# Kernel optimization log

Measured on AMD Instinct MI355X. Metric: run time of the kernel, lower is better.

Reference implementation:

```python
import jax, jax.numpy as jnp
import numpy as np

B = 131072
GI, GO = 4, 4          # input/output pathway groups
NI, NO = 64, 32        # neurons per input group (256/4), per output group (128/4)


def _gelu(t):
    # torch F.gelu default = exact erf gelu
    return jax.nn.gelu(t, approximate=False)


def setup_inputs() -> dict:
    key = jax.random.key(0)
    ks = jax.random.split(key, 16)
    s = 0.02
    return {
        "x":  jax.random.normal(ks[0], (B, 784), jnp.float32),
        "W1": jax.random.normal(ks[1], (512, 784), jnp.float32) * s,
        "b1": jax.random.normal(ks[2], (512,), jnp.float32) * s,
        "W2": jax.random.normal(ks[3], (256, 512), jnp.float32) * s,
        "b2": jax.random.normal(ks[4], (256,), jnp.float32) * s,
        "W3": jax.random.normal(ks[5], (128, 256), jnp.float32) * s,
        "b3": jax.random.normal(ks[6], (128,), jnp.float32) * s,
        "W4": jax.random.normal(ks[7], (64, 128), jnp.float32) * s,
        "b4": jax.random.normal(ks[8], (64,), jnp.float32) * s,
        "W5": jax.random.normal(ks[9], (32, 64), jnp.float32) * s,
        "b5": jax.random.normal(ks[10], (32,), jnp.float32) * s,
        "W6": jax.random.normal(ks[11], (10, 32), jnp.float32) * s,
        "b6": jax.random.normal(ks[12], (10,), jnp.float32) * s,
        "Wr": jax.random.normal(ks[13], (GI * GO, 256), jnp.float32) * s,
        "br": jax.random.normal(ks[14], (GI * GO,), jnp.float32) * s,
    }


def reference(x, W1, b1, W2, b2, W3, b3, W4, b4, W5, b5, W6, b6, Wr, br):
    # pre-middle dense chain (middle_layer == 3)
    h = _gelu(x @ W1.T + b1)          # [B, 512]
    mid_in = _gelu(h @ W2.T + b2)     # [B, 256]

    # router over 16 pathways; pathway_idx = i*GO + j -> reshape [B, GI, GO]
    pw = jax.nn.softmax(mid_in @ Wr.T + br, axis=-1).reshape(-1, GI, GO)

    # grouped pathway matmuls on fc3 (contiguous neuron groups -> reshape)
    xi = mid_in.reshape(-1, GI, NI)            # [B, GI, NI]
    W3g = W3.reshape(GO, NO, GI, NI)           # [GO, NO, GI, NI]
    part = jnp.einsum('bgi,ongi->bgon', xi, W3g)            # [B, GI, GO, NO]
    part = part + b3.reshape(GO, NO)[None, None]            # bias per pathway
    mid_out = jnp.einsum('bgo,bgon->bon', pw, part).reshape(-1, GO * NO)  # [B,128]
    mid_out = _gelu(mid_out)

    # post-middle dense chain
    h = _gelu(mid_out @ W4.T + b4)    # [B, 64]
    h = _gelu(h @ W5.T + b5)          # [B, 32]
    return h @ W6.T + b6              # [B, 10]
```

## Files before the change

kernel.cpp:

```cpp
#include <hip/hip_runtime.h>
#include <cstdint>

typedef _Float16 f16;
typedef _Float16 f16x4 __attribute__((ext_vector_type(4)));
typedef _Float16 f16x8 __attribute__((ext_vector_type(8)));
typedef float f32x4 __attribute__((ext_vector_type(4)));

#define MFMA16(a, b, c) __builtin_amdgcn_mfma_f32_16x16x32_f16((a), (b), (c), 0, 0, 0)

__device__ __forceinline__ float gelu_f(float x) {
    return 0.5f * x * (1.0f + erff(x * 0.70710678118654752440f));
}

__device__ __forceinline__ void load_lds16(const void* g, void* l) {
    __builtin_amdgcn_global_load_lds(
        (const __attribute__((address_space(1))) void*)(uintptr_t)g,
        (__attribute__((address_space(3))) void*)(uint32_t)(uintptr_t)l,
        16, 0, 0);
}

__global__ void k_prep(const float* __restrict__ W1, const float* __restrict__ W2,
                       const float* __restrict__ W3, const float* __restrict__ W4,
                       const float* __restrict__ W5, const float* __restrict__ W6,
                       const float* __restrict__ Wr,
                       f16* __restrict__ W1p, f16* __restrict__ W2f, f16* __restrict__ W3f,
                       f16* __restrict__ W4f, f16* __restrict__ W5f, f16* __restrict__ W6p,
                       f16* __restrict__ Wrf) {
    int i = blockIdx.x * 256 + threadIdx.x;
    if (i < 409600) {
        int r = i / 800, c = i - r * 800;
        W1p[i] = (f16)(c < 784 ? W1[r * 784 + c] : 0.0f);
        return;
    }
    i -= 409600;
    if (i < 131072) { W2f[i] = (f16)W2[i]; return; }
    i -= 131072;
    if (i < 32768) { W3f[i] = (f16)W3[i]; return; }
    i -= 32768;
    if (i < 8192) { W4f[i] = (f16)W4[i]; return; }
    i -= 8192;
    if (i < 2048) { W5f[i] = (f16)W5[i]; return; }
    i -= 2048;
    if (i < 512) {
        int r = i >> 5, c = i & 31;
        W6p[i] = (f16)(r < 10 ? W6[r * 32 + c] : 0.0f);
        return;
    }
    i -= 512;
    if (i < 4096) { Wrf[i] = (f16)Wr[i]; return; }
}

__global__ __launch_bounds__(256)
void k_xcvt(const float* __restrict__ X, f16* __restrict__ X16) {
    const size_t t = (size_t)blockIdx.x * 256 + threadIdx.x;
    const size_t row = t / 200;
    const int c4 = (int)(t - row * 200) * 4;
    f16x4 v = {0, 0, 0, 0};
    if (c4 < 784) {
        const float4 f = *(const float4*)(X + row * 784 + c4);
        v[0] = (f16)f.x; v[1] = (f16)f.y; v[2] = (f16)f.z; v[3] = (f16)f.w;
    }
    *(f16x4*)(X16 + row * 800 + c4) = v;
}

__global__ __launch_bounds__(256, 2)
void k_gemm1(const f16* __restrict__ A, const f16* __restrict__ Bw,
             const float* __restrict__ bias, f16* __restrict__ C) {
    __shared__ f16 As[128 * 32];
    __shared__ f16 Bs[256 * 32];
    const int tid = threadIdx.x;
    const int wave = tid >> 6, lane = tid & 63;
    const int nt = blockIdx.x & 1;
    const size_t mt = blockIdx.x >> 1;
    const size_t row0 = mt * 128;
    const int col0 = nt * 256;
    const int am = lane & 15, akg = lane >> 4, ak = akg * 8;
    const int wm = (wave & 1) * 64, wn = (wave >> 1) * 128;
    const f32x4 zero4 = {0.f, 0.f, 0.f, 0.f};
    f32x4 acc[4][8];
#pragma unroll
    for (int i = 0; i < 4; ++i)
#pragma unroll
        for (int j = 0; j < 8; ++j) acc[i][j] = zero4;

    const int srow = lane >> 2;
    const int scol = (lane & 3) * 8;

    for (int kt = 0; kt < 25; ++kt) {
        const int kb = kt * 32;
#pragma unroll
        for (int i = 0; i < 2; ++i) {
            const int inst = wave * 2 + i;
            load_lds16(A + (row0 + inst * 16 + srow) * 800 + kb + scol, &As[inst * 512]);
        }
#pragma unroll
        for (int i = 0; i < 4; ++i) {
            const int inst = wave * 4 + i;
            load_lds16(Bw + (size_t)(col0 + inst * 16 + srow) * 800 + kb + scol, &Bs[inst * 512]);
        }
        __syncthreads();
        f16x8 af[4], bf[8];
#pragma unroll
        for (int i = 0; i < 4; ++i) af[i] = *(const f16x8*)&As[(wm + i * 16 + am) * 32 + ak];
#pragma unroll
        for (int j = 0; j < 8; ++j) bf[j] = *(const f16x8*)&Bs[(wn + j * 16 + am) * 32 + ak];
#pragma unroll
        for (int i = 0; i < 4; ++i)
#pragma unroll
            for (int j = 0; j < 8; ++j)
                acc[i][j] = MFMA16(af[i], bf[j], acc[i][j]);
        __syncthreads();
    }
    const int cr = akg * 4;
#pragma unroll
    for (int j = 0; j < 8; ++j) {
        const int col = col0 + wn + j * 16 + am;
        const float b = bias[col];
#pragma unroll
        for (int i = 0; i < 4; ++i) {
            const size_t row = row0 + wm + i * 16 + cr;
#pragma unroll
            for (int r = 0; r < 4; ++r)
                C[(row + r) * 512 + col] = (f16)gelu_f(acc[i][j][r] + b);
        }
    }
}

__global__ __launch_bounds__(256, 2)
void k_gemm2(const f16* __restrict__ A, const f16* __restrict__ Bw,
             const float* __restrict__ bias, f16* __restrict__ C) {
    __shared__ f16 As[128 * 32];
    __shared__ f16 Bs[256 * 32];
    const int tid = threadIdx.x;
    const int wave = tid >> 6, lane = tid & 63;
    const size_t row0 = (size_t)blockIdx.x * 128;
    const int am = lane & 15, akg = lane >> 4, ak = akg * 8;
    const int wm = (wave & 1) * 64, wn = (wave >> 1) * 128;
    const f32x4 zero4 = {0.f, 0.f, 0.f, 0.f};
    f32x4 acc[4][8];
#pragma unroll
    for (int i = 0; i < 4; ++i)
#pragma unroll
        for (int j = 0; j < 8; ++j) acc[i][j] = zero4;

    const int srow = lane >> 2;
    const int scol = (lane & 3) * 8;

    for (int kt = 0; kt < 16; ++kt) {
        const int kb = kt * 32;
#pragma unroll
        for (int i = 0; i < 2; ++i) {
            const int inst = wave * 2 + i;
            load_lds16(A + (row0 + inst * 16 + srow) * 512 + kb + scol, &As[inst * 512]);
        }
#pragma unroll
        for (int i = 0; i < 4; ++i) {
            const int inst = wave * 4 + i;
            load_lds16(Bw + (size_t)(inst * 16 + srow) * 512 + kb + scol, &Bs[inst * 512]);
        }
        __syncthreads();
        f16x8 af[4], bf[8];
#pragma unroll
        for (int i = 0; i < 4; ++i) af[i] = *(const f16x8*)&As[(wm + i * 16 + am) * 32 + ak];
#pragma unroll
        for (int j = 0; j < 8; ++j) bf[j] = *(const f16x8*)&Bs[(wn + j * 16 + am) * 32 + ak];
#pragma unroll
        for (int i = 0; i < 4; ++i)
#pragma unroll
            for (int j = 0; j < 8; ++j)
                acc[i][j] = MFMA16(af[i], bf[j], acc[i][j]);
        __syncthreads();
    }
    const int cr = akg * 4;
#pragma unroll
    for (int j = 0; j < 8; ++j) {
        const int col = wn + j * 16 + am;
        const float b = bias[col];
#pragma unroll
        for (int i = 0; i < 4; ++i) {
            const size_t row = row0 + wm + i * 16 + cr;
#pragma unroll
            for (int r = 0; r < 4; ++r)
                C[(row + r) * 256 + col] = (f16)gelu_f(acc[i][j][r] + b);
        }
    }
}

__global__ __launch_bounds__(256, 2)
void k_tail(const f16* __restrict__ MID,
            const f16* __restrict__ W3f, const float* __restrict__ b3,
            const f16* __restrict__ W4f, const float* __restrict__ b4,
            const f16* __restrict__ W5f, const float* __restrict__ b5,
            const f16* __restrict__ W6p, const float* __restrict__ b6v,
            const f16* __restrict__ Wrf, const float* __restrict__ brv,
            float* __restrict__ OUT) {
    __shared__ f16 s_mid[64 * 264];
    __shared__ float s_pw[64 * 20];
    __shared__ f16 s_mo[64 * 136];
    __shared__ f16 s_h4[64 * 72];
    __shared__ f16 s_h5[64 * 40];
    const int tid = threadIdx.x, wave = tid >> 6, lane = tid & 63;
    const size_t r0 = (size_t)blockIdx.x * 64;
    const int am = lane & 15, akg = lane >> 4, ak = akg * 8;
    const int wr = wave * 16;
    const int crow = wr + akg * 4;
    const f32x4 zero4 = {0.f, 0.f, 0.f, 0.f};

    {
        const int row = tid >> 2, seg = (tid & 3) * 64;
        const f16* src = MID + (r0 + row) * 256 + seg;
        f16* dst = s_mid + row * 264 + seg;
#pragma unroll
        for (int c = 0; c < 8; ++c)
            *(f16x8*)(dst + c * 8) = *(const f16x8*)(src + c * 8);
    }
    __syncthreads();

    {
        f32x4 lacc = zero4;
#pragma unroll
        for (int ks = 0; ks < 8; ++ks) {
            f16x8 a = *(const f16x8*)(s_mid + (wr + am) * 264 + ks * 32 + ak);
            f16x8 b = *(const f16x8*)(Wrf + am * 256 + ks * 32 + ak);
            lacc = MFMA16(a, b, lacc);
        }
        const float brn = brv[am];
#pragma unroll
        for (int r = 0; r < 4; ++r) {
            float l = lacc[r] + brn;
            float mx = l;
#pragma unroll
            for (int m = 1; m <= 8; m <<= 1) mx = fmaxf(mx, __shfl_xor(mx, m));
            const float e = __expf(l - mx);
            float s = e;
#pragma unroll
            for (int m = 1; m <= 8; m <<= 1) s += __shfl_xor(s, m);
            const float p = e / s;
            float sg = p;
            sg += __shfl_xor(sg, 4);
            sg += __shfl_xor(sg, 8);
            s_pw[(crow + r) * 20 + am] = p;
            if (am < 4) s_pw[(crow + r) * 20 + 16 + am] = sg;
        }
    }
    __syncthreads();

    {
        f16x8 a3[4][2];
#pragma unroll
        for (int g = 0; g < 4; ++g)
#pragma unroll
            for (int kh = 0; kh < 2; ++kh)
                a3[g][kh] = *(const f16x8*)(s_mid + (wr + am) * 264 + g * 64 + kh * 32 + ak);
#pragma unroll
        for (int o = 0; o < 4; ++o) {
            float pwv[4][4], sgl[4];
#pragma unroll
            for (int r = 0; r < 4; ++r) {
                sgl[r] = s_pw[(crow + r) * 20 + 16 + o];
#pragma unroll
                for (int g = 0; g < 4; ++g)
                    pwv[g][r] = s_pw[(crow + r) * 20 + g * 4 + o];
            }
#pragma unroll
            for (int ctl = 0; ctl < 2; ++ctl) {
                const int ct = o * 2 + ctl;
                const int col = ct * 16 + am;
                const float bias = b3[col];
                f32x4 oacc;
#pragma unroll
                for (int r = 0; r < 4; ++r) oacc[r] = bias * sgl[r];
#pragma unroll
                for (int g = 0; g < 4; ++g) {
                    f32x4 t = zero4;
                    t = MFMA16(a3[g][0], *(const f16x8*)(W3f + (size_t)col * 256 + g * 64 + ak), t);
                    t = MFMA16(a3[g][1], *(const f16x8*)(W3f + (size_t)col * 256 + g * 64 + 32 + ak), t);
#pragma unroll
                    for (int r = 0; r < 4; ++r) oacc[r] += pwv[g][r] * t[r];
                }
#pragma unroll
                for (int r = 0; r < 4; ++r)
                    s_mo[(crow + r) * 136 + col] = (f16)gelu_f(oacc[r]);
            }
        }
    }
    __syncthreads();

    {
        f16x8 a4[4];
#pragma unroll
        for (int ks = 0; ks < 4; ++ks)
            a4[ks] = *(const f16x8*)(s_mo + (wr + am) * 136 + ks * 32 + ak);
#pragma unroll
        for (int ct = 0; ct < 4; ++ct) {
            const int col = ct * 16 + am;
            f32x4 acc = zero4;
#pragma unroll
            for (int ks = 0; ks < 4; ++ks)
                acc = MFMA16(a4[ks], *(const f16x8*)(W4f + (size_t)col * 128 + ks * 32 + ak), acc);
            const float bias = b4[col];
#pragma unroll
            for (int r = 0; r < 4; ++r)
                s_h4[(crow + r) * 72 + col] = (f16)gelu_f(acc[r] + bias);
        }
    }
    __syncthreads();

    {
        f16x8 a5[2];
#pragma unroll
        for (int ks = 0; ks < 2; ++ks)
            a5[ks] = *(const f16x8*)(s_h4 + (wr + am) * 72 + ks * 32 + ak);
#pragma unroll
        for (int ct = 0; ct < 2; ++ct) {
            const int col = ct * 16 + am;
            f32x4 acc = zero4;
#pragma unroll
            for (int ks = 0; ks < 2; ++ks)
                acc = MFMA16(a5[ks], *(const f16x8*)(W5f + (size_t)col * 64 + ks * 32 + ak), acc);
            const float bias = b5[col];
#pragma unroll
            for (int r = 0; r < 4; ++r)
                s_h5[(crow + r) * 40 + col] = (f16)gelu_f(acc[r] + bias);
        }
    }
    __syncthreads();

    {
        f16x8 a6 = *(const f16x8*)(s_h5 + (wr + am) * 40 + ak);
        f16x8 bw = *(const f16x8*)(W6p + am * 32 + ak);
        f32x4 acc = MFMA16(a6, bw, zero4);
        if (am < 10) {
            const float bb = b6v[am];
#pragma unroll
            for (int r = 0; r < 4; ++r)
                OUT[(r0 + crow + r) * 10 + am] = acc[r] + bb;
        }
    }
}

extern "C" void kernel_launch(void* const* d_in, const int* in_sizes, int n_in,
                              void* d_out, int out_size, void* d_ws, size_t ws_size,
                              hipStream_t stream) {
    const float* x  = (const float*)d_in[0];
    const float* W1 = (const float*)d_in[1];
    const float* b1 = (const float*)d_in[2];
    const float* W2 = (const float*)d_in[3];
    const float* b2 = (const float*)d_in[4];
    const float* W3 = (const float*)d_in[5];
    const float* b3 = (const float*)d_in[6];
    const float* W4 = (const float*)d_in[7];
    const float* b4 = (const float*)d_in[8];
    const float* W5 = (const float*)d_in[9];
    const float* b5 = (const float*)d_in[10];
    const float* W6 = (const float*)d_in[11];
    const float* b6 = (const float*)d_in[12];
    const float* Wr = (const float*)d_in[13];
    const float* br = (const float*)d_in[14];
    float* out = (float*)d_out;

    const int M = in_sizes[0] / 784;

    char* ws = (char*)d_ws;
    f16* W1p = (f16*)ws; ws += 512 * 800 * 2;
    f16* W2f = (f16*)ws; ws += 256 * 512 * 2;
    f16* W3f = (f16*)ws; ws += 128 * 256 * 2;
    f16* W4f = (f16*)ws; ws += 64 * 128 * 2;
    f16* W5f = (f16*)ws; ws += 32 * 64 * 2;
    f16* W6p = (f16*)ws; ws += 16 * 32 * 2;
    f16* Wrf = (f16*)ws; ws += 16 * 256 * 2;
    f16* X16 = (f16*)ws;
    f16* MIDB = (f16*)ws; ws += (size_t)M * 800 * 2;
    f16* H1  = (f16*)ws; ws += (size_t)M * 512 * 2;

    k_prep<<<2298, 256, 0, stream>>>(W1, W2, W3, W4, W5, W6, Wr,
                                     W1p, W2f, W3f, W4f, W5f, W6p, Wrf);
    k_xcvt<<<(M * 200) / 256, 256, 0, stream>>>(x, X16);
    k_gemm1<<<(M / 128) * 2, 256, 0, stream>>>(X16, W1p, b1, H1);
    k_gemm2<<<M / 128, 256, 0, stream>>>(H1, W2f, b2, MIDB);
    k_tail<<<M / 64, 256, 0, stream>>>(MIDB, W3f, b3, W4f, b4, W5f, b5,
                                       W6p, b6, Wrf, br, out);
}
```

Baseline: 985.3 us.

## Use K=64 tiles, swapped MFMA operands for vector stores, and tanh-form GELU

The GEMM kernels now load two 32-wide K slabs per barrier pair, which halves the number of synchronizations and packs more MFMAs between barriers. K padding grows from 800 to 832 to match. Swapping the MFMA operands transposes the accumulator layout, so the epilogue can do float4 bias loads and f16x4 vectorized stores instead of scattered scalar stores. The exact erf GELU is replaced by a sigmoid/tanh approximation using exp and rcp, which lowers epilogue cost but adds approximation error, and LDS use doubles.

```diff
diff --git a/kernel.cpp b/kernel.cpp
--- a/kernel.cpp
+++ b/kernel.cpp
@@ -9,7 +9,8 @@
 #define MFMA16(a, b, c) __builtin_amdgcn_mfma_f32_16x16x32_f16((a), (b), (c), 0, 0, 0)
 
 __device__ __forceinline__ float gelu_f(float x) {
-    return 0.5f * x * (1.0f + erff(x * 0.70710678118654752440f));
+    const float u = x * (1.5957691216f + 0.0713548163f * x * x);
+    return x * __builtin_amdgcn_rcpf(1.0f + __expf(-u));
 }
 
 __device__ __forceinline__ void load_lds16(const void* g, void* l) {
@@ -27,12 +28,12 @@
                        f16* __restrict__ W4f, f16* __restrict__ W5f, f16* __restrict__ W6p,
                        f16* __restrict__ Wrf) {
     int i = blockIdx.x * 256 + threadIdx.x;
-    if (i < 409600) {
-        int r = i / 800, c = i - r * 800;
+    if (i < 425984) {
+        int r = i / 832, c = i - r * 832;
         W1p[i] = (f16)(c < 784 ? W1[r * 784 + c] : 0.0f);
         return;
     }
-    i -= 409600;
+    i -= 425984;
     if (i < 131072) { W2f[i] = (f16)W2[i]; return; }
     i -= 131072;
     if (i < 32768) { W3f[i] = (f16)W3[i]; return; }
@@ -53,21 +54,21 @@
 __global__ __launch_bounds__(256)
 void k_xcvt(const float* __restrict__ X, f16* __restrict__ X16) {
     const size_t t = (size_t)blockIdx.x * 256 + threadIdx.x;
-    const size_t row = t / 200;
-    const int c4 = (int)(t - row * 200) * 4;
+    const size_t row = t / 208;
+    const int c4 = (int)(t - row * 208) * 4;
     f16x4 v = {0, 0, 0, 0};
     if (c4 < 784) {
         const float4 f = *(const float4*)(X + row * 784 + c4);
         v[0] = (f16)f.x; v[1] = (f16)f.y; v[2] = (f16)f.z; v[3] = (f16)f.w;
     }
-    *(f16x4*)(X16 + row * 800 + c4) = v;
+    *(f16x4*)(X16 + row * 832 + c4) = v;
 }
 
 __global__ __launch_bounds__(256, 2)
 void k_gemm1(const f16* __restrict__ A, const f16* __restrict__ Bw,
              const float* __restrict__ bias, f16* __restrict__ C) {
-    __shared__ f16 As[128 * 32];
-    __shared__ f16 Bs[256 * 32];
+    __shared__ f16 As[2 * 128 * 32];
+    __shared__ f16 Bs[2 * 256 * 32];
     const int tid = threadIdx.x;
     const int wave = tid >> 6, lane = tid & 63;
     const int nt = blockIdx.x & 1;
@@ -86,42 +87,55 @@
     const int srow = lane >> 2;
     const int scol = (lane & 3) * 8;
 
-    for (int kt = 0; kt < 25; ++kt) {
-        const int kb = kt * 32;
-#pragma unroll
-        for (int i = 0; i < 2; ++i) {
-            const int inst = wave * 2 + i;
-            load_lds16(A + (row0 + inst * 16 + srow) * 800 + kb + scol, &As[inst * 512]);
-        }
-#pragma unroll
-        for (int i = 0; i < 4; ++i) {
-            const int inst = wave * 4 + i;
-            load_lds16(Bw + (size_t)(col0 + inst * 16 + srow) * 800 + kb + scol, &Bs[inst * 512]);
+    for (int kt = 0; kt < 13; ++kt) {
+        const int kb = kt * 64;
+#pragma unroll
+        for (int p = 0; p < 2; ++p) {
+#pragma unroll
+            for (int i = 0; i < 2; ++i) {
+                const int inst = wave * 2 + i;
+                load_lds16(A + (row0 + inst * 16 + srow) * 832 + kb + p * 32 + scol,
+                           &As[p * 4096 + inst * 512]);
+            }
+#pragma unroll
+            for (int i = 0; i < 4; ++i) {
+                const int inst = wave * 4 + i;
+                load_lds16(Bw + (size_t)(col0 + inst * 16 + srow) * 832 + kb + p * 32 + scol,
+                           &Bs[p * 8192 + inst * 512]);
+            }
         }
         __syncthreads();
-        f16x8 af[4], bf[8];
-#pragma unroll
-        for (int i = 0; i < 4; ++i) af[i] = *(const f16x8*)&As[(wm + i * 16 + am) * 32 + ak];
-#pragma unroll
-        for (int j = 0; j < 8; ++j) bf[j] = *(const f16x8*)&Bs[(wn + j * 16 + am) * 32 + ak];
-#pragma unroll
-        for (int i = 0; i < 4; ++i)
+#pragma unroll
+        for (int ks = 0; ks < 2; ++ks) {
+            f16x8 af[4], bf[8];
+#pragma unroll
+            for (int i = 0; i < 4; ++i)
+                af[i] = *(const f16x8*)&As[ks * 4096 + (wm + i * 16 + am) * 32 + ak];
 #pragma unroll
             for (int j = 0; j < 8; ++j)
-                acc[i][j] = MFMA16(af[i], bf[j], acc[i][j]);
+                bf[j] = *(const f16x8*)&Bs[ks * 8192 + (wn + j * 16 + am) * 32 + ak];
+#pragma unroll
+            for (int i = 0; i < 4; ++i)
+#pragma unroll
+                for (int j = 0; j < 8; ++j)
+                    acc[i][j] = MFMA16(bf[j], af[i], acc[i][j]);
+        }
         __syncthreads();
     }
-    const int cr = akg * 4;
-#pragma unroll
-    for (int j = 0; j < 8; ++j) {
-        const int col = col0 + wn + j * 16 + am;
-        const float b = bias[col];
-#pragma unroll
-        for (int i = 0; i < 4; ++i) {
-            const size_t row = row0 + wm + i * 16 + cr;
-#pragma unroll
-            for (int r = 0; r < 4; ++r)
-                C[(row + r) * 512 + col] = (f16)gelu_f(acc[i][j][r] + b);
+    const int cc = akg * 4;
+#pragma unroll
+    for (int i = 0; i < 4; ++i) {
+        const size_t row = row0 + wm + i * 16 + am;
+#pragma unroll
+        for (int j = 0; j < 8; ++j) {
+            const int col = col0 + wn + j * 16 + cc;
+            const float4 b4 = *(const float4*)(bias + col);
+            f16x4 v;
+            v[0] = (f16)gelu_f(acc[i][j][0] + b4.x);
+            v[1] = (f16)gelu_f(acc[i][j][1] + b4.y);
+            v[2] = (f16)gelu_f(acc[i][j][2] + b4.z);
+            v[3] = (f16)gelu_f(acc[i][j][3] + b4.w);
+            *(f16x4*)(C + row * 512 + col) = v;
         }
     }
 }
@@ -129,8 +143,8 @@
 __global__ __launch_bounds__(256, 2)
 void k_gemm2(const f16* __restrict__ A, const f16* __restrict__ Bw,
              const float* __restrict__ bias, f16* __restrict__ C) {
-    __shared__ f16 As[128 * 32];
-    __shared__ f16 Bs[256 * 32];
+    __shared__ f16 As[2 * 128 * 32];
+    __shared__ f16 Bs[2 * 256 * 32];
     const int tid = threadIdx.x;
     const int wave = tid >> 6, lane = tid & 63;
     const size_t row0 = (size_t)blockIdx.x * 128;
@@ -146,42 +160,55 @@
     const int srow = lane >> 2;
     const int scol = (lane & 3) * 8;
 
-    for (int kt = 0; kt < 16; ++kt) {
-        const int kb = kt * 32;
-#pragma unroll
-        for (int i = 0; i < 2; ++i) {
-            const int inst = wave * 2 + i;
-            load_lds16(A + (row0 + inst * 16 + srow) * 512 + kb + scol, &As[inst * 512]);
-        }
-#pragma unroll
-        for (int i = 0; i < 4; ++i) {
-            const int inst = wave * 4 + i;
-            load_lds16(Bw + (size_t)(inst * 16 + srow) * 512 + kb + scol, &Bs[inst * 512]);
+    for (int kt = 0; kt < 8; ++kt) {
+        const int kb = kt * 64;
+#pragma unroll
+        for (int p = 0; p < 2; ++p) {
+#pragma unroll
+            for (int i = 0; i < 2; ++i) {
+                const int inst = wave * 2 + i;
+                load_lds16(A + (row0 + inst * 16 + srow) * 512 + kb + p * 32 + scol,
+                           &As[p * 4096 + inst * 512]);
+            }
+#pragma unroll
+            for (int i = 0; i < 4; ++i) {
+                const int inst = wave * 4 + i;
+                load_lds16(Bw + (size_t)(inst * 16 + srow) * 512 + kb + p * 32 + scol,
+                           &Bs[p * 8192 + inst * 512]);
+            }
         }
         __syncthreads();
-        f16x8 af[4], bf[8];
-#pragma unroll
-        for (int i = 0; i < 4; ++i) af[i] = *(const f16x8*)&As[(wm + i * 16 + am) * 32 + ak];
-#pragma unroll
-        for (int j = 0; j < 8; ++j) bf[j] = *(const f16x8*)&Bs[(wn + j * 16 + am) * 32 + ak];
-#pragma unroll
-        for (int i = 0; i < 4; ++i)
+#pragma unroll
+        for (int ks = 0; ks < 2; ++ks) {
+            f16x8 af[4], bf[8];
+#pragma unroll
+            for (int i = 0; i < 4; ++i)
+                af[i] = *(const f16x8*)&As[ks * 4096 + (wm + i * 16 + am) * 32 + ak];
 #pragma unroll
             for (int j = 0; j < 8; ++j)
-                acc[i][j] = MFMA16(af[i], bf[j], acc[i][j]);
+                bf[j] = *(const f16x8*)&Bs[ks * 8192 + (wn + j * 16 + am) * 32 + ak];
+#pragma unroll
+            for (int i = 0; i < 4; ++i)
+#pragma unroll
+                for (int j = 0; j < 8; ++j)
+                    acc[i][j] = MFMA16(bf[j], af[i], acc[i][j]);
+        }
         __syncthreads();
     }
-    const int cr = akg * 4;
-#pragma unroll
-    for (int j = 0; j < 8; ++j) {
-        const int col = wn + j * 16 + am;
-        const float b = bias[col];
-#pragma unroll
-        for (int i = 0; i < 4; ++i) {
-            const size_t row = row0 + wm + i * 16 + cr;
-#pragma unroll
-            for (int r = 0; r < 4; ++r)
-                C[(row + r) * 256 + col] = (f16)gelu_f(acc[i][j][r] + b);
+    const int cc = akg * 4;
+#pragma unroll
+    for (int i = 0; i < 4; ++i) {
+        const size_t row = row0 + wm + i * 16 + am;
+#pragma unroll
+        for (int j = 0; j < 8; ++j) {
+            const int col = wn + j * 16 + cc;
+            const float4 b4 = *(const float4*)(bias + col);
+            f16x4 v;
+            v[0] = (f16)gelu_f(acc[i][j][0] + b4.x);
+            v[1] = (f16)gelu_f(acc[i][j][1] + b4.y);
+            v[2] = (f16)gelu_f(acc[i][j][2] + b4.z);
+            v[3] = (f16)gelu_f(acc[i][j][3] + b4.w);
+            *(f16x4*)(C + row * 256 + col) = v;
         }
     }
 }
@@ -362,7 +389,7 @@
     const int M = in_sizes[0] / 784;
 
     char* ws = (char*)d_ws;
-    f16* W1p = (f16*)ws; ws += 512 * 800 * 2;
+    f16* W1p = (f16*)ws; ws += 512 * 832 * 2;
     f16* W2f = (f16*)ws; ws += 256 * 512 * 2;
     f16* W3f = (f16*)ws; ws += 128 * 256 * 2;
     f16* W4f = (f16*)ws; ws += 64 * 128 * 2;
@@ -370,12 +397,12 @@
     f16* W6p = (f16*)ws; ws += 16 * 32 * 2;
     f16* Wrf = (f16*)ws; ws += 16 * 256 * 2;
     f16* X16 = (f16*)ws;
-    f16* MIDB = (f16*)ws; ws += (size_t)M * 800 * 2;
+    f16* MIDB = (f16*)ws; ws += (size_t)M * 832 * 2;
     f16* H1  = (f16*)ws; ws += (size_t)M * 512 * 2;
 
-    k_prep<<<2298, 256, 0, stream>>>(W1, W2, W3, W4, W5, W6, Wr,
+    k_prep<<<2362, 256, 0, stream>>>(W1, W2, W3, W4, W5, W6, Wr,
                                      W1p, W2f, W3f, W4f, W5f, W6p, Wrf);
-    k_xcvt<<<(M * 200) / 256, 256, 0, stream>>>(x, X16);
+    k_xcvt<<<(M * 208) / 256, 256, 0, stream>>>(x, X16);
     k_gemm1<<<(M / 128) * 2, 256, 0, stream>>>(X16, W1p, b1, H1);
     k_gemm2<<<M / 128, 256, 0, stream>>>(H1, W2f, b2, MIDB);
     k_tail<<<M / 64, 256, 0, stream>>>(MIDB, W3f, b3, W4f, b4, W5f, b5,
```

New measurement: 906.5 us. 1.09x faster.
